# Kernel optimization log

Measured on AMD Instinct MI355X. Metric: run time of the kernel, lower is better.

Reference implementation:

```python
import jax, jax.numpy as jnp
import numpy as np
import math

B, N, CS, CZ = 2, 512, 384, 128
H, C, PQ, PV = 12, 16, 4, 8
EPS = 1e-8

def _quat_to_rot(q):
    q = q / jnp.linalg.norm(q, axis=-1, keepdims=True)
    a, b, c, d = q[..., 0], q[..., 1], q[..., 2], q[..., 3]
    return jnp.stack([
        jnp.stack([a*a+b*b-c*c-d*d, 2*(b*c-a*d), 2*(b*d+a*c)], -1),
        jnp.stack([2*(b*c+a*d), a*a-b*b+c*c-d*d, 2*(c*d-a*b)], -1),
        jnp.stack([2*(b*d-a*c), 2*(c*d+a*b), a*a-b*b-c*c+d*d], -1)], -2)

def setup_inputs() -> dict:
    key = jax.random.key(0)
    ks = jax.random.split(key, 12)
    def lin(k, out_f, in_f):
        return jax.random.normal(k, (out_f, in_f), jnp.float32) * math.sqrt(1.0 / in_f)
    inp = {}
    inp['single'] = jax.random.normal(ks[0], (B, N, CS), jnp.float32)
    inp['pair'] = jax.random.normal(ks[1], (B, N, N, CZ), jnp.float32)
    inp['rotations'] = _quat_to_rot(jax.random.normal(ks[2], (B, N, 4), jnp.float32))
    inp['translations'] = jax.random.normal(ks[3], (B, N, 3), jnp.float32) * 10.0
    inp['wq'] = lin(ks[4], H*C, CS); inp['bq'] = jnp.zeros((H*C,), jnp.float32)
    inp['wkv'] = lin(ks[5], 2*H*C, CS); inp['bkv'] = jnp.zeros((2*H*C,), jnp.float32)
    inp['wqp'] = lin(ks[6], 3*H*PQ, CS); inp['bqp'] = jnp.zeros((3*H*PQ,), jnp.float32)
    inp['wkvp'] = lin(ks[7], 3*H*(PQ+PV), CS); inp['bkvp'] = jnp.zeros((3*H*(PQ+PV),), jnp.float32)
    inp['wb'] = lin(ks[8], H, CZ); inp['bb'] = jnp.zeros((H,), jnp.float32)
    out_in = H*C + H*PV*4 + H*CZ  # scalar + (x,y,z,norm) points + pair
    inp['wo'] = lin(ks[9], CS, out_in); inp['bo'] = jnp.zeros((CS,), jnp.float32)
    inp['head_weights'] = jax.random.normal(ks[10], (H,), jnp.float32) * 0.1
    return inp

def _ipa(single, pair, rotations, translations, wq, bq, wkv, bkv, wqp, bqp, wkvp, bkvp, wb, bb, wo, bo, head_weights):
    b_, n_ = single.shape[0], single.shape[1]
    # scalar q/k/v
    q = (single @ wq.T + bq).reshape(b_, n_, H, C)
    kv = (single @ wkv.T + bkv).reshape(b_, n_, H, 2*C)
    k, v = kv[..., :C], kv[..., C:]
    # point q/k/v in local frames (chunk into x,y,z then stack, per _project_points)
    def proj_pts(w, bvec, P):
        raw = single @ w.T + bvec
        xc, yc, zc = jnp.split(raw, 3, axis=-1)
        return jnp.stack([xc, yc, zc], -1).reshape(b_, n_, H, P, 3)
    q_pts = proj_pts(wqp, bqp, PQ)
    kv_pts = proj_pts(wkvp, bkvp, PQ + PV)
    k_pts, v_pts = kv_pts[..., :PQ, :], kv_pts[..., PQ:, :]
    # apply rigid frames: global = R @ p + t
    def to_global(p):
        return jnp.einsum('biop,bihqp->bihqo', rotations, p) + translations[:, :, None, None, :]
    qg, kg, vg = to_global(q_pts), to_global(k_pts), to_global(v_pts)
    # scalar logits + pair bias
    bias = pair @ wb.T + bb  # [B,N,N,H]
    logits = jnp.einsum('bihc,bjhc->bhij', q, k) * math.sqrt(1.0 / (3.0 * C))
    logits = logits + math.sqrt(1.0 / 3.0) * bias.transpose(0, 3, 1, 2)
    # point-distance logits
    d2 = jnp.sum((qg[:, :, None] - kg[:, None]) ** 2, axis=-1)  # [B,N,N,H,PQ]
    gamma = jax.nn.softplus(head_weights)  # [H]
    wpt = math.sqrt(1.0 / (3.0 * PQ * 4.5))
    pt_logits = -0.5 * wpt * jnp.sum(d2, axis=-1) * gamma  # [B,N,N,H]
    attn = jax.nn.softmax(logits + pt_logits.transpose(0, 3, 1, 2), axis=-1)  # [B,H,N,N]
    # assemble output features
    out_scalar = jnp.einsum('bhij,bjhc->bihc', attn, v).reshape(b_, n_, H*C)
    rp_g = jnp.einsum('bhij,bjhpc->bihpc', attn, vg)
    # back to local frame: R^T @ (p - t)
    rp_l = jnp.einsum('bipo,bihqp->bihqo', rotations, rp_g - translations[:, :, None, None, :])
    norms = jnp.sqrt(jnp.sum(rp_l ** 2, -1) + EPS).reshape(b_, n_, H*PV)
    rp_l = rp_l.reshape(b_, n_, H*PV, 3)
    out_pair = jnp.einsum('bhij,bijd->bihd', attn, pair).reshape(b_, n_, H*CZ)
    feats = jnp.concatenate([out_scalar, rp_l[..., 0], rp_l[..., 1], rp_l[..., 2], norms, out_pair], -1)
    return feats @ wo.T + bo

def reference(single, pair, rotations, translations, wq, bq, wkv, bkv, wqp, bqp, wkvp, bkvp, wb, bb, wo, bo, head_weights):
    return _ipa(single, pair, rotations, translations, wq, bq, wkv, bkv, wqp, bqp, wkvp, bkvp, wb, bb, wo, bo, head_weights)
```

## Files before the change

kernel.cpp:

```cpp
#include <hip/hip_runtime.h>
#include <hip/hip_bf16.h>
#include <math.h>

#define NB 2
#define NN 512
#define CSD 384
#define CZD 128
#define NH 12
#define NC 16
#define NPQ 4
#define NPV 8
#define HC 192
#define QPDIM 144
#define FEATD 2112
#define WPT 0.13608276348795434f
#define RS3C 0.14433756729740643f
#define RS3 0.5773502691896258f

typedef __attribute__((ext_vector_type(8))) short short8;
typedef __attribute__((ext_vector_type(4))) float f32x4;

static __device__ inline unsigned short f2bf(float x) {
    __hip_bfloat16 h = __float2bfloat16(x);
    return *reinterpret_cast<unsigned short*>(&h);
}
static __device__ inline unsigned short bflo(float x) {
    __hip_bfloat16 h = __float2bfloat16(x);
    return f2bf(x - __bfloat162float(h));
}

#define R_S0 393216
#define R_S1 (R_S0 + 73728)
#define R_S2 (R_S1 + 147456)
#define R_S3 (R_S2 + 55296)
#define R_S4 (R_S3 + 165888)
#define R_S5 (R_S4 + 811008)
#define R_S6 (R_S5 + 2048)
__global__ __launch_bounds__(256) void k_cvt(
    const float* __restrict__ single, const float* __restrict__ wq,
    const float* __restrict__ wkv, const float* __restrict__ wqp,
    const float* __restrict__ wkvp, const float* __restrict__ wo,
    const float* __restrict__ wb,
    unsigned short* __restrict__ singleb, unsigned short* __restrict__ wallb,
    unsigned short* __restrict__ wob, unsigned short* __restrict__ wbb)
{
    int gid = blockIdx.x * 256 + threadIdx.x;
    int e = gid * 4;
    if (e >= R_S6) return;
    if (e >= R_S5) {
        int c = e - R_S5;
        int hh = c >> 7;
        ushort4 o;
        if (hh < 12) {
            float4 v = *(const float4*)(wb + hh * 128 + (c & 127));
            o.x = f2bf(v.x); o.y = f2bf(v.y); o.z = f2bf(v.z); o.w = f2bf(v.w);
        } else { o.x = 0; o.y = 0; o.z = 0; o.w = 0; }
        *(ushort4*)(wbb + c) = o;
        return;
    }
    const float* src; unsigned short* dst;
    if (e < R_S0)      { src = single + e;          dst = singleb + e; }
    else if (e < R_S1) { src = wq + (e - R_S0);     dst = wallb + (e - R_S0); }
    else if (e < R_S2) { src = wkv + (e - R_S1);    dst = wallb + 73728 + (e - R_S1); }
    else if (e < R_S3) { src = wqp + (e - R_S2);    dst = wallb + 221184 + (e - R_S2); }
    else if (e < R_S4) { src = wkvp + (e - R_S3);   dst = wallb + 276480 + (e - R_S3); }
    else               { src = wo + (e - R_S4);     dst = wob + (e - R_S4); }
    float4 v = *(const float4*)src;
    ushort4 o;
    o.x = f2bf(v.x); o.y = f2bf(v.y); o.z = f2bf(v.z); o.w = f2bf(v.w);
    *(ushort4*)dst = o;
}

__global__ __launch_bounds__(256) void k_gemm1(
    const unsigned short* __restrict__ A, const unsigned short* __restrict__ Bm,
    float* __restrict__ Cr)
{
    int w = threadIdx.x >> 6, lane = threadIdx.x & 63;
    int rt = blockIdx.x;
    int ct = blockIdx.y * 4 + w;
    int r = lane & 15, kq = lane >> 4;
    const unsigned short* ap = A  + (size_t)(rt * 16 + r) * 384 + kq * 8;
    const unsigned short* bp = Bm + (size_t)(ct * 16 + r) * 384 + kq * 8;
    f32x4 acc = {0.f, 0.f, 0.f, 0.f};
    #pragma unroll 4
    for (int ks = 0; ks < 12; ++ks) {
        short8 av = *(const short8*)(ap + ks * 32);
        short8 bv = *(const short8*)(bp + ks * 32);
        acc = __builtin_amdgcn_mfma_f32_16x16x32_bf16(av, bv, acc, 0, 0, 0);
    }
    int crow = rt * 16 + kq * 4;
    int ccol = ct * 16 + r;
    #pragma unroll
    for (int i = 0; i < 4; ++i)
        Cr[(size_t)(crow + i) * 1152 + ccol] = acc[i];
}

__global__ __launch_bounds__(256) void k_post(
    const float* __restrict__ praw, const float* __restrict__ rot, const float* __restrict__ trans,
    const float* __restrict__ hw,
    const float* __restrict__ bq, const float* __restrict__ bkv,
    const float* __restrict__ bqp, const float* __restrict__ bkvp,
    unsigned short* __restrict__ vallT2,
    unsigned short* __restrict__ qhat, unsigned short* __restrict__ khat,
    float* __restrict__ qn2, float* __restrict__ kn2)
{
    __shared__ float s_q[192], s_k[192], s_v[192], s_qp[QPDIM], s_kvp[432];
    __shared__ float s_qg[144], s_kg[144], s_vg[288];
    __shared__ float s_sh[12];
    const int t = threadIdx.x;
    const int row = blockIdx.x;
    const int b = row >> 9;
    const int i = row & 511;

    if (t < 12) {
        float sp = log1pf(expf(hw[t]));
        s_sh[t] = RS3C / (WPT * sp);
    }
    const float* pr = praw + (size_t)row * 1152;
    for (int idx = t; idx < 1152; idx += 256) {
        float v = pr[idx];
        if (idx < 192) {
            s_q[idx] = v + bq[idx];
        } else if (idx < 576) {
            int f = idx - 192; float x = v + bkv[f];
            int h = f >> 5, cc = f & 31;
            if (cc < 16) s_k[h * 16 + cc] = x;
            else         s_v[h * 16 + cc - 16] = x;
        } else if (idx < 720) {
            int f = idx - 576; s_qp[f] = v + bqp[f];
        } else {
            int f = idx - 720; s_kvp[f] = v + bkvp[f];
        }
    }
    __syncthreads();

    if (t < 192) {
        const float* R = rot + (size_t)row * 9;
        const float* T = trans + (size_t)row * 3;
        float lx, ly, lz; float* dst;
        if (t < 48) {
            lx = s_qp[t]; ly = s_qp[48 + t]; lz = s_qp[96 + t];
            dst = s_qg + t * 3;
        } else if (t < 96) {
            int idx = t - 48; int fb = (idx >> 2) * 12 + (idx & 3);
            lx = s_kvp[fb]; ly = s_kvp[144 + fb]; lz = s_kvp[288 + fb];
            dst = s_kg + idx * 3;
        } else {
            int idx = t - 96; int fb = (idx >> 3) * 12 + 4 + (idx & 7);
            lx = s_kvp[fb]; ly = s_kvp[144 + fb]; lz = s_kvp[288 + fb];
            dst = s_vg + idx * 3;
        }
        dst[0] = R[0] * lx + R[1] * ly + R[2] * lz + T[0];
        dst[1] = R[3] * lx + R[4] * ly + R[5] * lz + T[1];
        dst[2] = R[6] * lx + R[7] * ly + R[8] * lz + T[2];
    }
    __syncthreads();

    if (t < 24) {
        int h = t % 12;
        const float* g = (t < 12) ? (s_qg + h * 12) : (s_kg + h * 12);
        float s = 0.f;
        #pragma unroll
        for (int e = 0; e < 12; ++e) s += g[e] * g[e];
        float* dst = (t < 12) ? qn2 : kn2;
        dst[((size_t)b * 12 + h) * 512 + i] = s;
    }

    for (int c = t; c < 768; c += 256) {
        int h = c >> 6, cp = c & 63;
        unsigned short v;
        if (cp < 16)      v = f2bf(s_v[h * 16 + cp]);
        else if (cp < 40) v = f2bf(s_vg[h * 24 + cp - 16]);
        else              v = bflo(s_vg[h * 24 + cp - 40]);
        vallT2[((size_t)(b * 12 + h) * 64 + cp) * 512 + i] = v;
    }

    for (int idx = t; idx < 768; idx += 256) {
        int side = idx >= 384;
        int li = side ? (idx - 384) : idx;
        int h = li >> 5, s2 = li & 31;
        unsigned short o[2];
        #pragma unroll
        for (int u = 0; u < 2; ++u) {
            int k = 2 * s2 + u;
            unsigned short val = 0;
            if (!side) {
                if (k < 16)      val = f2bf(s_sh[h] * s_q[h * 16 + k]);
                else if (k < 28) val = f2bf(s_qg[h * 12 + k - 16]);
                else if (k < 40) val = f2bf(s_qg[h * 12 + k - 28]);
                else if (k < 52) val = bflo(s_qg[h * 12 + k - 40]);
            } else {
                if (k < 16)      val = f2bf(s_k[h * 16 + k]);
                else if (k < 28) val = f2bf(s_kg[h * 12 + k - 16]);
                else if (k < 40) val = bflo(s_kg[h * 12 + k - 28]);
                else if (k < 52) val = f2bf(s_kg[h * 12 + k - 40]);
            }
            o[u] = val;
        }
        unsigned short* dst = (side ? khat : qhat) + (((size_t)b * 12 + h) * 512 + i) * 64 + 2 * s2;
        *(ushort2*)dst = make_ushort2(o[0], o[1]);
    }
}

__global__ __launch_bounds__(256) void k_qk(
    const unsigned short* __restrict__ qhat, const unsigned short* __restrict__ khat,
    const float* __restrict__ qn2, const float* __restrict__ kn2,
    const float* __restrict__ hw, float* __restrict__ plog)
{
    int w = threadIdx.x >> 6, lane = threadIdx.x & 63;
    int bh = blockIdx.x;
    int i0 = (blockIdx.y >> 3) * 64;
    int j0 = (blockIdx.y & 7) * 64;
    int r = lane & 15, kq = lane >> 4;
    float sp = log1pf(expf(hw[bh % 12]));
    float m = WPT * sp;
    float coef = -0.5f * m;

    const unsigned short* ap = qhat + ((size_t)bh * 512 + i0 + w * 16 + r) * 64 + kq * 8;
    short8 a0 = *(const short8*)(ap);
    short8 a1 = *(const short8*)(ap + 32);
    const unsigned short* bpb = khat + ((size_t)bh * 512 + j0 + r) * 64 + kq * 8;
    f32x4 acc[4];
    #pragma unroll
    for (int jt = 0; jt < 4; ++jt) {
        short8 b0 = *(const short8*)(bpb + (size_t)jt * 1024);
        short8 b1 = *(const short8*)(bpb + (size_t)jt * 1024 + 32);
        f32x4 a = {0.f, 0.f, 0.f, 0.f};
        a = __builtin_amdgcn_mfma_f32_16x16x32_bf16(a0, b0, a, 0, 0, 0);
        a = __builtin_amdgcn_mfma_f32_16x16x32_bf16(a1, b1, a, 0, 0, 0);
        acc[jt] = a;
    }
    int crow = i0 + w * 16 + kq * 4;
    const float* qn = qn2 + (size_t)bh * 512;
    const float* kn = kn2 + (size_t)bh * 512;
    #pragma unroll
    for (int jt = 0; jt < 4; ++jt) {
        int ccol = j0 + jt * 16 + r;
        float knv = kn[ccol];
        #pragma unroll
        for (int ii = 0; ii < 4; ++ii)
            plog[((size_t)bh * 512 + crow + ii) * 512 + ccol] =
                m * acc[jt][ii] + coef * (qn[crow + ii] + knv);
    }
}

__global__ __launch_bounds__(512) void k_av(
    const float* __restrict__ pair,
    const unsigned short* __restrict__ wbb, const float* __restrict__ bb,
    const float* __restrict__ plog,
    unsigned short* __restrict__ attnb, unsigned short* __restrict__ featsb)
{
    __shared__ __align__(16) unsigned char smem_raw[34816];
    float (*attn12)[521] = (float(*)[521])smem_raw;
    unsigned short* ldsT = (unsigned short*)smem_raw;

    const int t = threadIdx.x;
    const int row_i = blockIdx.x;
    const int b = row_i >> 9;
    const int i_loc = row_i & 511;
    const int w = t >> 6, lane = t & 63;
    const int r = lane & 15, kq = lane >> 4;

    {
        const unsigned short* bp = wbb + r * 128 + kq * 8;
        short8 bfrag[4];
        #pragma unroll
        for (int ks = 0; ks < 4; ++ks) bfrag[ks] = *(const short8*)(bp + ks * 32);
        float bbv = (r < 12) ? bb[r] : 0.f;
        #pragma unroll
        for (int tt = 0; tt < 4; ++tt) {
            int tile = w + tt * 8;
            const float* ap = pair + ((size_t)row_i * NN + tile * 16 + r) * CZD + kq * 8;
            float4 p[8];
            #pragma unroll
            for (int ks = 0; ks < 4; ++ks) {
                p[2 * ks]     = *(const float4*)(ap + ks * 32);
                p[2 * ks + 1] = *(const float4*)(ap + ks * 32 + 4);
            }
            f32x4 acc = {0.f, 0.f, 0.f, 0.f};
            #pragma unroll
            for (int ks = 0; ks < 4; ++ks) {
                short8 av;
                av[0] = (short)f2bf(p[2*ks].x);   av[1] = (short)f2bf(p[2*ks].y);
                av[2] = (short)f2bf(p[2*ks].z);   av[3] = (short)f2bf(p[2*ks].w);
                av[4] = (short)f2bf(p[2*ks+1].x); av[5] = (short)f2bf(p[2*ks+1].y);
                av[6] = (short)f2bf(p[2*ks+1].z); av[7] = (short)f2bf(p[2*ks+1].w);
                acc = __builtin_amdgcn_mfma_f32_16x16x32_bf16(av, bfrag[ks], acc, 0, 0, 0);
            }
            if (r < 12) {
                #pragma unroll
                for (int ii = 0; ii < 4; ++ii)
                    attn12[r][tile * 16 + kq * 4 + ii] = RS3 * (acc[ii] + bbv);
            }
        }
    }
    __syncthreads();

    #pragma unroll
    for (int it = 0; it < 3; ++it) {
        int idx4 = it * 512 + t;
        int h = idx4 >> 7;
        int j4 = (idx4 & 127) * 4;
        const float* lp = plog + (((size_t)b * 12 + h) * 512 + i_loc) * 512 + j4;
        float4 lv = *(const float4*)lp;
        attn12[h][j4 + 0] += lv.x;
        attn12[h][j4 + 1] += lv.y;
        attn12[h][j4 + 2] += lv.z;
        attn12[h][j4 + 3] += lv.w;
    }
    __syncthreads();

    for (int hh = w; hh < 12; hh += 8) {
        float vreg[8];
        float mx = -1e30f;
        #pragma unroll
        for (int s = 0; s < 8; ++s) { vreg[s] = attn12[hh][lane + 64 * s]; mx = fmaxf(mx, vreg[s]); }
        #pragma unroll
        for (int off = 32; off >= 1; off >>= 1) mx = fmaxf(mx, __shfl_xor(mx, off, 64));
        float ssum = 0.f;
        #pragma unroll
        for (int s = 0; s < 8; ++s) { vreg[s] = __expf(vreg[s] - mx); ssum += vreg[s]; }
        #pragma unroll
        for (int off = 32; off >= 1; off >>= 1) ssum += __shfl_xor(ssum, off, 64);
        float inv = 1.0f / ssum;
        #pragma unroll
        for (int s = 0; s < 8; ++s) attn12[hh][lane + 64 * s] = vreg[s] * inv;
    }
    __syncthreads();

    for (int idx = t; idx < 768; idx += 512) {
        int h = idx >> 6, jc = idx & 63;
        ushort4 o0, o1;
        o0.x = f2bf(attn12[h][jc * 8 + 0]); o0.y = f2bf(attn12[h][jc * 8 + 1]);
        o0.z = f2bf(attn12[h][jc * 8 + 2]); o0.w = f2bf(attn12[h][jc * 8 + 3]);
        o1.x = f2bf(attn12[h][jc * 8 + 4]); o1.y = f2bf(attn12[h][jc * 8 + 5]);
        o1.z = f2bf(attn12[h][jc * 8 + 6]); o1.w = f2bf(attn12[h][jc * 8 + 7]);
        unsigned short* gp = attnb + (((size_t)(b * 12 + h) * 512 + i_loc)) * 512 + jc * 8;
        *(ushort4*)gp = o0;
        *(ushort4*)(gp + 4) = o1;
    }
    __syncthreads();

    {
        const int d0 = w * 16;
        const int hr = (r < 12) ? r : 11;
        const unsigned short* arow = attnb + (((size_t)(b * 12 + hr) * 512 + i_loc)) * 512 + kq * 8;
        const int jl = t >> 2, dq = t & 3;
        const float* srcb = pair + (size_t)row_i * NN * CZD + dq * 32;
        f32x4 acc = {0.f, 0.f, 0.f, 0.f};
        for (int st = 0; st < 4; ++st) {
            const float* src = srcb + (size_t)(st * 128 + jl) * CZD;
            float4 vv[8];
            #pragma unroll
            for (int u = 0; u < 8; ++u) vv[u] = *(const float4*)(src + u * 4);
            #pragma unroll
            for (int u = 0; u < 8; ++u) {
                int d = dq * 32 + u * 4;
                ldsT[(size_t)(d + 0) * 136 + jl] = f2bf(vv[u].x);
                ldsT[(size_t)(d + 1) * 136 + jl] = f2bf(vv[u].y);
                ldsT[(size_t)(d + 2) * 136 + jl] = f2bf(vv[u].z);
                ldsT[(size_t)(d + 3) * 136 + jl] = f2bf(vv[u].w);
            }
            __syncthreads();
            #pragma unroll
            for (int ks = 0; ks < 4; ++ks) {
                short8 av = *(const short8*)(arow + st * 128 + ks * 32);
                short8 bv = *(const short8*)(ldsT + (size_t)(d0 + r) * 136 + ks * 32 + kq * 8);
                acc = __builtin_amdgcn_mfma_f32_16x16x32_bf16(av, bv, acc, 0, 0, 0);
            }
            __syncthreads();
        }
        unsigned short* frow = featsb + (size_t)row_i * FEATD;
        if (kq < 3) {
            #pragma unroll
            for (int ii = 0; ii < 4; ++ii) {
                int h = kq * 4 + ii;
                frow[576 + h * CZD + d0 + r] = f2bf(acc[ii]);
            }
        }
    }
}

__global__ __launch_bounds__(512) void k_avg(
    const unsigned short* __restrict__ attnb, const unsigned short* __restrict__ vallT2,
    const float* __restrict__ rot, const float* __restrict__ trans,
    unsigned short* __restrict__ featsb)
{
    __shared__ float rp_s[32][49];
    int bh = blockIdx.x;
    int itile = blockIdx.y;
    int b = bh / 12, h = bh % 12;
    int t = threadIdx.x;
    int w = t >> 6, lane = t & 63;
    int mt = w >> 2, nt = w & 3;
    int r = lane & 15, kq = lane >> 4;
    int i0 = itile * 32 + mt * 16;
    const unsigned short* ap = attnb + ((size_t)bh * 512 + i0 + r) * 512 + kq * 8;
    const unsigned short* bp = vallT2 + ((size_t)bh * 64 + nt * 16 + r) * 512 + kq * 8;
    f32x4 acc = {0.f, 0.f, 0.f, 0.f};
    #pragma unroll
    for (int ks = 0; ks < 16; ++ks) {
        short8 av = *(const short8*)(ap + ks * 32);
        short8 bv = *(const short8*)(bp + ks * 32);
        acc = __builtin_amdgcn_mfma_f32_16x16x32_bf16(av, bv, acc, 0, 0, 0);
    }
    int cp = nt * 16 + r;
    #pragma unroll
    for (int ii = 0; ii < 4; ++ii) {
        int il = mt * 16 + kq * 4 + ii;
        if (nt == 0) {
            size_t rowg = (size_t)b * 512 + itile * 32 + il;
            featsb[rowg * FEATD + h * 16 + r] = f2bf(acc[ii]);
        } else {
            rp_s[il][cp - 16] = acc[ii];
        }
    }
    __syncthreads();
    if (t < 256) {
        int il = t >> 3, p = t & 7;
        size_t rowg = (size_t)b * 512 + itile * 32 + il;
        const float* R = rot + rowg * 9;
        const float* T = trans + rowg * 3;
        float g0 = rp_s[il][p * 3 + 0] + rp_s[il][24 + p * 3 + 0];
        float g1 = rp_s[il][p * 3 + 1] + rp_s[il][24 + p * 3 + 1];
        float g2 = rp_s[il][p * 3 + 2] + rp_s[il][24 + p * 3 + 2];
        float d0 = g0 - T[0], d1 = g1 - T[1], d2v = g2 - T[2];
        float l0 = R[0] * d0 + R[3] * d1 + R[6] * d2v;
        float l1 = R[1] * d0 + R[4] * d1 + R[7] * d2v;
        float l2 = R[2] * d0 + R[5] * d1 + R[8] * d2v;
        float nrm = sqrtf(l0 * l0 + l1 * l1 + l2 * l2 + 1e-8f);
        unsigned short* frow = featsb + rowg * FEATD;
        int hp = h * 8 + p;
        frow[192 + hp] = f2bf(l0);
        frow[288 + hp] = f2bf(l1);
        frow[384 + hp] = f2bf(l2);
        frow[480 + hp] = f2bf(nrm);
    }
}

__global__ __launch_bounds__(256) void k_gemm2(
    const unsigned short* __restrict__ A, const unsigned short* __restrict__ Bm,
    const float* __restrict__ bo, float* __restrict__ out)
{
    int w = threadIdx.x >> 6, lane = threadIdx.x & 63;
    int rt = blockIdx.x;
    int ct = blockIdx.y * 4 + w;
    int r = lane & 15, kq = lane >> 4;
    const unsigned short* ap = A  + (size_t)(rt * 16 + r) * FEATD + kq * 8;
    const unsigned short* bp = Bm + (size_t)(ct * 16 + r) * FEATD + kq * 8;
    f32x4 acc = {0.f, 0.f, 0.f, 0.f};
    #pragma unroll 2
    for (int ks = 0; ks < 66; ++ks) {
        short8 av = *(const short8*)(ap + ks * 32);
        short8 bv = *(const short8*)(bp + ks * 32);
        acc = __builtin_amdgcn_mfma_f32_16x16x32_bf16(av, bv, acc, 0, 0, 0);
    }
    int crow = rt * 16 + kq * 4;
    int ccol = ct * 16 + r;
    float bv = bo[ccol];
    #pragma unroll
    for (int i = 0; i < 4; ++i)
        out[(size_t)(crow + i) * CSD + ccol] = acc[i] + bv;
}

extern "C" void kernel_launch(void* const* d_in, const int* in_sizes, int n_in,
                              void* d_out, int out_size, void* d_ws, size_t ws_size,
                              hipStream_t stream) {
    const float* single = (const float*)d_in[0];
    const float* pair   = (const float*)d_in[1];
    const float* rot    = (const float*)d_in[2];
    const float* trans  = (const float*)d_in[3];
    const float* wq     = (const float*)d_in[4];
    const float* bq     = (const float*)d_in[5];
    const float* wkv    = (const float*)d_in[6];
    const float* bkv    = (const float*)d_in[7];
    const float* wqp    = (const float*)d_in[8];
    const float* bqp    = (const float*)d_in[9];
    const float* wkvp   = (const float*)d_in[10];
    const float* bkvp   = (const float*)d_in[11];
    const float* wb     = (const float*)d_in[12];
    const float* bb     = (const float*)d_in[13];
    const float* wo     = (const float*)d_in[14];
    const float* bo     = (const float*)d_in[15];
    const float* hw     = (const float*)d_in[16];
    float* out = (float*)d_out;

    float* ws = (float*)d_ws;
    float* plog    = ws;
    float* projraw = ws;
    unsigned short* qhat = (unsigned short*)(ws + 6291456);
    unsigned short* khat = (unsigned short*)(ws + 6684672);
    float* qn2     = ws + 7077888;
    float* kn2     = ws + 7090176;
    unsigned short* featsb  = (unsigned short*)(ws + 7102464);
    unsigned short* singleb = (unsigned short*)(ws + 8183808);
    unsigned short* wallb   = (unsigned short*)(ws + 8380416);
    unsigned short* wob     = (unsigned short*)(ws + 8601600);
    unsigned short* wbb     = (unsigned short*)(ws + 9007104);
    unsigned short* vallT2  = (unsigned short*)(ws + 9008128);
    unsigned short* attnb   = (unsigned short*)(ws + 9401344);

    hipLaunchKernelGGL(k_cvt, dim3(1610), dim3(256), 0, stream,
                       single, wq, wkv, wqp, wkvp, wo, wb, singleb, wallb, wob, wbb);
    hipLaunchKernelGGL(k_gemm1, dim3(64, 18), dim3(256), 0, stream, singleb, wallb, projraw);
    hipLaunchKernelGGL(k_post, dim3(1024), dim3(256), 0, stream,
                       projraw, rot, trans, hw, bq, bkv, bqp, bkvp,
                       vallT2, qhat, khat, qn2, kn2);
    hipLaunchKernelGGL(k_qk, dim3(24, 64), dim3(256), 0, stream,
                       qhat, khat, qn2, kn2, hw, plog);
    hipLaunchKernelGGL(k_av, dim3(1024), dim3(512), 0, stream,
                       pair, wbb, bb, plog, attnb, featsb);
    hipLaunchKernelGGL(k_avg, dim3(24, 16), dim3(512), 0, stream,
                       attnb, vallT2, rot, trans, featsb);
    hipLaunchKernelGGL(k_gemm2, dim3(64, 6), dim3(256), 0, stream, featsb, wob, bo, out);
}
```

Before: 202.3 us.

## Restage pair tile in k_av with larger LDS stages and swizzled vector stores

After: 203.9 us. Within noise of the previous version (+0.8%).

```diff
diff --git a/kernel.cpp b/kernel.cpp
--- a/kernel.cpp
+++ b/kernel.cpp
@@ -250,7 +250,7 @@
     const float* __restrict__ plog,
     unsigned short* __restrict__ attnb, unsigned short* __restrict__ featsb)
 {
-    __shared__ __align__(16) unsigned char smem_raw[34816];
+    __shared__ __align__(16) unsigned char smem_raw[67584];
     float (*attn12)[521] = (float(*)[521])smem_raw;
     unsigned short* ldsT = (unsigned short*)smem_raw;
 
@@ -344,31 +344,45 @@
     {
         const int d0 = w * 16;
         const int hr = (r < 12) ? r : 11;
-        const unsigned short* arow = attnb + (((size_t)(b * 12 + hr) * 512 + i_loc)) * 512 + kq * 8;
-        const int jl = t >> 2, dq = t & 3;
-        const float* srcb = pair + (size_t)row_i * NN * CZD + dq * 32;
+        const unsigned short* arow = attnb + (((size_t)(b * 12 + hr) * 512 + i_loc)) * 512;
+        const int dg = t & 7;
+        const int jq = t >> 3;
+        const int j0l = jq * 4;
         f32x4 acc = {0.f, 0.f, 0.f, 0.f};
-        for (int st = 0; st < 4; ++st) {
-            const float* src = srcb + (size_t)(st * 128 + jl) * CZD;
-            float4 vv[8];
+        for (int stage = 0; stage < 2; ++stage) {
+            const float* srcs = pair + (size_t)row_i * NN * CZD
+                              + (size_t)(stage * 256 + j0l) * CZD + dg * 16;
+            if (stage == 1) __syncthreads();
             #pragma unroll
-            for (int u = 0; u < 8; ++u) vv[u] = *(const float4*)(src + u * 4);
-            #pragma unroll
-            for (int u = 0; u < 8; ++u) {
-                int d = dq * 32 + u * 4;
-                ldsT[(size_t)(d + 0) * 136 + jl] = f2bf(vv[u].x);
-                ldsT[(size_t)(d + 1) * 136 + jl] = f2bf(vv[u].y);
-                ldsT[(size_t)(d + 2) * 136 + jl] = f2bf(vv[u].z);
-                ldsT[(size_t)(d + 3) * 136 + jl] = f2bf(vv[u].w);
+            for (int u = 0; u < 4; ++u) {
+                float4 v0 = *(const float4*)(srcs + 0 * CZD + u * 4);
+                float4 v1 = *(const float4*)(srcs + 1 * CZD + u * 4);
+                float4 v2 = *(const float4*)(srcs + 2 * CZD + u * 4);
+                float4 v3 = *(const float4*)(srcs + 3 * CZD + u * 4);
+                const float* f0 = (const float*)&v0;
+                const float* f1 = (const float*)&v1;
+                const float* f2 = (const float*)&v2;
+                const float* f3 = (const float*)&v3;
+                #pragma unroll
+                for (int e = 0; e < 4; ++e) {
+                    int d = dg * 16 + u * 4 + e;
+                    ushort4 ov;
+                    ov.x = f2bf(f0[e]); ov.y = f2bf(f1[e]);
+                    ov.z = f2bf(f2[e]); ov.w = f2bf(f3[e]);
+                    int idx = d * 264 + j0l;
+                    idx ^= ((d >> 4) & 7) << 4;
+                    *(ushort4*)(ldsT + idx) = ov;
+                }
             }
             __syncthreads();
             #pragma unroll
-            for (int ks = 0; ks < 4; ++ks) {
-                short8 av = *(const short8*)(arow + st * 128 + ks * 32);
-                short8 bv = *(const short8*)(ldsT + (size_t)(d0 + r) * 136 + ks * 32 + kq * 8);
+            for (int ks = 0; ks < 8; ++ks) {
+                short8 av = *(const short8*)(arow + stage * 256 + ks * 32 + kq * 8);
+                int idx = (d0 + r) * 264 + ks * 32 + kq * 8;
+                idx ^= (((d0 + r) >> 4) & 7) << 4;
+                short8 bv = *(const short8*)(ldsT + idx);
                 acc = __builtin_amdgcn_mfma_f32_16x16x32_bf16(av, bv, acc, 0, 0, 0);
             }
-            __syncthreads();
         }
         unsigned short* frow = featsb + (size_t)row_i * FEATD;
         if (kq < 3) {
```

## Split pair-weighted attention output into separate kernel with direct-register loads

Applied to the files above, without the earlier changes.

Result: no change. 199.0 us (-1.6%).

```diff
diff --git a/kernel.cpp b/kernel.cpp
--- a/kernel.cpp
+++ b/kernel.cpp
@@ -244,15 +244,13 @@
     }
 }
 
-__global__ __launch_bounds__(512) void k_av(
+__global__ __launch_bounds__(512) void k_av2(
     const float* __restrict__ pair,
     const unsigned short* __restrict__ wbb, const float* __restrict__ bb,
     const float* __restrict__ plog,
-    unsigned short* __restrict__ attnb, unsigned short* __restrict__ featsb)
-{
-    __shared__ __align__(16) unsigned char smem_raw[34816];
-    float (*attn12)[521] = (float(*)[521])smem_raw;
-    unsigned short* ldsT = (unsigned short*)smem_raw;
+    unsigned short* __restrict__ attnb)
+{
+    __shared__ float attn12[12][521];
 
     const int t = threadIdx.x;
     const int row_i = blockIdx.x;
@@ -339,44 +337,48 @@
         *(ushort4*)gp = o0;
         *(ushort4*)(gp + 4) = o1;
     }
-    __syncthreads();
-
-    {
-        const int d0 = w * 16;
-        const int hr = (r < 12) ? r : 11;
-        const unsigned short* arow = attnb + (((size_t)(b * 12 + hr) * 512 + i_loc)) * 512 + kq * 8;
-        const int jl = t >> 2, dq = t & 3;
-        const float* srcb = pair + (size_t)row_i * NN * CZD + dq * 32;
-        f32x4 acc = {0.f, 0.f, 0.f, 0.f};
-        for (int st = 0; st < 4; ++st) {
-            const float* src = srcb + (size_t)(st * 128 + jl) * CZD;
-            float4 vv[8];
-            #pragma unroll
-            for (int u = 0; u < 8; ++u) vv[u] = *(const float4*)(src + u * 4);
-            #pragma unroll
-            for (int u = 0; u < 8; ++u) {
-                int d = dq * 32 + u * 4;
-                ldsT[(size_t)(d + 0) * 136 + jl] = f2bf(vv[u].x);
-                ldsT[(size_t)(d + 1) * 136 + jl] = f2bf(vv[u].y);
-                ldsT[(size_t)(d + 2) * 136 + jl] = f2bf(vv[u].z);
-                ldsT[(size_t)(d + 3) * 136 + jl] = f2bf(vv[u].w);
-            }
-            __syncthreads();
-            #pragma unroll
-            for (int ks = 0; ks < 4; ++ks) {
-                short8 av = *(const short8*)(arow + st * 128 + ks * 32);
-                short8 bv = *(const short8*)(ldsT + (size_t)(d0 + r) * 136 + ks * 32 + kq * 8);
-                acc = __builtin_amdgcn_mfma_f32_16x16x32_bf16(av, bv, acc, 0, 0, 0);
-            }
-            __syncthreads();
-        }
-        unsigned short* frow = featsb + (size_t)row_i * FEATD;
-        if (kq < 3) {
-            #pragma unroll
-            for (int ii = 0; ii < 4; ++ii) {
-                int h = kq * 4 + ii;
-                frow[576 + h * CZD + d0 + r] = f2bf(acc[ii]);
-            }
+}
+
+__global__ __launch_bounds__(256) void k_op(
+    const float* __restrict__ pair, const unsigned short* __restrict__ attnb,
+    unsigned short* __restrict__ featsb)
+{
+    const int t = threadIdx.x;
+    const int row_i = blockIdx.x;
+    const int dh = blockIdx.y;
+    const int b = row_i >> 9;
+    const int i_loc = row_i & 511;
+    const int w = t >> 6, lane = t & 63;
+    const int r = lane & 15, kq = lane >> 4;
+    const int d0 = (dh * 4 + w) * 16;
+    const int hr = (r < 12) ? r : 11;
+    const unsigned short* arow = attnb + ((size_t)(b * 12 + hr) * 512 + i_loc) * 512 + kq * 8;
+    const float* pbase = pair + (size_t)row_i * NN * CZD + d0 + r;
+    f32x4 acc = {0.f, 0.f, 0.f, 0.f};
+    for (int ks = 0; ks < 16; ++ks) {
+        int jb = ks * 32 + kq * 8;
+        float x0 = pbase[(size_t)(jb + 0) * CZD];
+        float x1 = pbase[(size_t)(jb + 1) * CZD];
+        float x2 = pbase[(size_t)(jb + 2) * CZD];
+        float x3 = pbase[(size_t)(jb + 3) * CZD];
+        float x4 = pbase[(size_t)(jb + 4) * CZD];
+        float x5 = pbase[(size_t)(jb + 5) * CZD];
+        float x6 = pbase[(size_t)(jb + 6) * CZD];
+        float x7 = pbase[(size_t)(jb + 7) * CZD];
+        short8 av = *(const short8*)(arow + ks * 32);
+        short8 bv;
+        bv[0] = (short)f2bf(x0); bv[1] = (short)f2bf(x1);
+        bv[2] = (short)f2bf(x2); bv[3] = (short)f2bf(x3);
+        bv[4] = (short)f2bf(x4); bv[5] = (short)f2bf(x5);
+        bv[6] = (short)f2bf(x6); bv[7] = (short)f2bf(x7);
+        acc = __builtin_amdgcn_mfma_f32_16x16x32_bf16(av, bv, acc, 0, 0, 0);
+    }
+    unsigned short* frow = featsb + (size_t)row_i * FEATD;
+    if (kq < 3) {
+        #pragma unroll
+        for (int ii = 0; ii < 4; ++ii) {
+            int h = kq * 4 + ii;
+            frow[576 + h * CZD + d0 + r] = f2bf(acc[ii]);
         }
     }
 }
@@ -508,8 +510,9 @@
                        vallT2, qhat, khat, qn2, kn2);
     hipLaunchKernelGGL(k_qk, dim3(24, 64), dim3(256), 0, stream,
                        qhat, khat, qn2, kn2, hw, plog);
-    hipLaunchKernelGGL(k_av, dim3(1024), dim3(512), 0, stream,
-                       pair, wbb, bb, plog, attnb, featsb);
+    hipLaunchKernelGGL(k_av2, dim3(1024), dim3(512), 0, stream,
+                       pair, wbb, bb, plog, attnb);
+    hipLaunchKernelGGL(k_op, dim3(1024, 2), dim3(256), 0, stream, pair, attnb, featsb);
     hipLaunchKernelGGL(k_avg, dim3(24, 16), dim3(512), 0, stream,
                        attnb, vallT2, rot, trans, featsb);
     hipLaunchKernelGGL(k_gemm2, dim3(64, 6), dim3(256), 0, stream, featsb, wob, bo, out);
```

## Give each wave a private double-buffered pair tile in k_av to drop block barriers

Applied to the files above, without the earlier changes.

New measurement: 185.5 us. -8.3%, faster.

```diff
diff --git a/kernel.cpp b/kernel.cpp
--- a/kernel.cpp
+++ b/kernel.cpp
@@ -250,9 +250,9 @@
     const float* __restrict__ plog,
     unsigned short* __restrict__ attnb, unsigned short* __restrict__ featsb)
 {
-    __shared__ __align__(16) unsigned char smem_raw[34816];
+    __shared__ __align__(16) unsigned char smem_raw[40960];
     float (*attn12)[521] = (float(*)[521])smem_raw;
-    unsigned short* ldsT = (unsigned short*)smem_raw;
+    unsigned short* opl = (unsigned short*)smem_raw;
 
     const int t = threadIdx.x;
     const int row_i = blockIdx.x;
@@ -345,30 +345,41 @@
         const int d0 = w * 16;
         const int hr = (r < 12) ? r : 11;
         const unsigned short* arow = attnb + (((size_t)(b * 12 + hr) * 512 + i_loc)) * 512 + kq * 8;
-        const int jl = t >> 2, dq = t & 3;
-        const float* srcb = pair + (size_t)row_i * NN * CZD + dq * 32;
+        unsigned short* wbuf = opl + w * 2560;
+        const int jr = lane >> 2;
+        const int dc = (lane & 3) * 4;
+        const float* psrc = pair + (size_t)row_i * NN * CZD + d0 + dc;
         f32x4 acc = {0.f, 0.f, 0.f, 0.f};
-        for (int st = 0; st < 4; ++st) {
-            const float* src = srcb + (size_t)(st * 128 + jl) * CZD;
-            float4 vv[8];
+
+        float4 bufr[2][4];
+        #pragma unroll
+        for (int u = 0; u < 4; ++u)
+            bufr[0][u] = *(const float4*)(psrc + (size_t)(jr + 16 * u) * CZD);
+
+        #pragma unroll
+        for (int ck = 0; ck < 8; ++ck) {
+            const int cb = ck & 1;
             #pragma unroll
-            for (int u = 0; u < 8; ++u) vv[u] = *(const float4*)(src + u * 4);
+            for (int u = 0; u < 4; ++u) {
+                float4 v = bufr[cb][u];
+                ushort4 s;
+                s.x = f2bf(v.x); s.y = f2bf(v.y); s.z = f2bf(v.z); s.w = f2bf(v.w);
+                *(ushort4*)(wbuf + cb * 1280 + (jr + 16 * u) * 20 + dc) = s;
+            }
+            if (ck < 7) {
+                #pragma unroll
+                for (int u = 0; u < 4; ++u)
+                    bufr[cb ^ 1][u] = *(const float4*)(psrc + (size_t)((ck + 1) * 64 + jr + 16 * u) * CZD);
+            }
             #pragma unroll
-            for (int u = 0; u < 8; ++u) {
-                int d = dq * 32 + u * 4;
-                ldsT[(size_t)(d + 0) * 136 + jl] = f2bf(vv[u].x);
-                ldsT[(size_t)(d + 1) * 136 + jl] = f2bf(vv[u].y);
-                ldsT[(size_t)(d + 2) * 136 + jl] = f2bf(vv[u].z);
-                ldsT[(size_t)(d + 3) * 136 + jl] = f2bf(vv[u].w);
-            }
-            __syncthreads();
-            #pragma unroll
-            for (int ks = 0; ks < 4; ++ks) {
-                short8 av = *(const short8*)(arow + st * 128 + ks * 32);
-                short8 bv = *(const short8*)(ldsT + (size_t)(d0 + r) * 136 + ks * 32 + kq * 8);
+            for (int mm = 0; mm < 2; ++mm) {
+                short8 bv;
+                #pragma unroll
+                for (int u = 0; u < 8; ++u)
+                    bv[u] = (short)wbuf[cb * 1280 + (mm * 32 + kq * 8 + u) * 20 + r];
+                short8 av = *(const short8*)(arow + ck * 64 + mm * 32);
                 acc = __builtin_amdgcn_mfma_f32_16x16x32_bf16(av, bv, acc, 0, 0, 0);
             }
-            __syncthreads();
         }
         unsigned short* frow = featsb + (size_t)row_i * FEATD;
         if (kq < 3) {
```
